# Kernel optimization log

Measured on AMD Instinct MI355X. Metric: run time of the kernel, lower is better.

## Reference

```python
import jax, jax.numpy as jnp
import numpy as np

N = 12288
IN_DIM = 256
HID = 64
E = 393216


def _gcn_edges(edge_index, n):
    # add self-loops, compute symmetric normalization (PyG GCNConv default)
    src = jnp.concatenate([edge_index[0], jnp.arange(n, dtype=edge_index.dtype)])
    dst = jnp.concatenate([edge_index[1], jnp.arange(n, dtype=edge_index.dtype)])
    deg = jax.ops.segment_sum(jnp.ones_like(src, dtype=jnp.float32), dst, num_segments=n)
    dinv = jnp.where(deg > 0, jax.lax.rsqrt(deg), 0.0)
    norm = dinv[src] * dinv[dst]  # [E+N]
    return src, dst, norm


def _conv(h, src, dst, norm, W, b, n):
    # GCNConv: linear transform then normalized sparse aggregation
    h = h @ W
    agg = jax.ops.segment_sum(h[src] * norm[:, None], dst, num_segments=n)
    return agg + b


def setup_inputs() -> dict:
    key = jax.random.key(0)
    ks = jax.random.split(key, 16)
    x = jax.random.normal(ks[0], (N, IN_DIM), dtype=jnp.float32)
    edge_index = jax.random.randint(ks[1], (2, E), 0, N, dtype=jnp.int32)
    s = 0.05
    p = {
        'enc_W1': jax.random.normal(ks[2], (IN_DIM, HID), jnp.float32) * s,
        'enc_b1': jnp.zeros((HID,), jnp.float32),
        'enc_W2': jax.random.normal(ks[3], (HID, HID), jnp.float32) * s,
        'enc_b2': jnp.zeros((HID,), jnp.float32),
        'd1_W1': jax.random.normal(ks[4], (HID // 2, HID), jnp.float32) * s,
        'd1_b1': jnp.zeros((HID,), jnp.float32),
        'd1_W2': jax.random.normal(ks[5], (HID, IN_DIM), jnp.float32) * s,
        'd1_b2': jnp.zeros((IN_DIM,), jnp.float32),
        'd2_W1': jax.random.normal(ks[6], (HID // 2, HID), jnp.float32) * s,
        'd2_b1': jnp.zeros((HID,), jnp.float32),
        'd2_W2': jax.random.normal(ks[7], (HID, IN_DIM), jnp.float32) * s,
        'd2_b2': jnp.zeros((IN_DIM,), jnp.float32),
        's_W': jax.random.normal(ks[8], (HID // 2, HID), jnp.float32) * s,
        's_b': jnp.zeros((HID,), jnp.float32),
    }
    return dict(x=x, edge_index=edge_index, **p)


def reference(x, edge_index, enc_W1, enc_b1, enc_W2, enc_b2,
              d1_W1, d1_b1, d1_W2, d1_b2, d2_W1, d2_b1, d2_W2, d2_b2,
              s_W, s_b):
    n = x.shape[0]
    src, dst, norm = _gcn_edges(edge_index, n)

    def encoder(h):
        h = jax.nn.relu(_conv(h, src, dst, norm, enc_W1, enc_b1, n))
        return _conv(h, src, dst, norm, enc_W2, enc_b2, n)

    def dec1(h):
        h = jax.nn.relu(_conv(h, src, dst, norm, d1_W1, d1_b1, n))
        return _conv(h, src, dst, norm, d1_W2, d1_b2, n)

    def dec2(h):
        h = jax.nn.relu(_conv(h, src, dst, norm, d2_W1, d2_b1, n))
        return _conv(h, src, dst, norm, d2_W2, d2_b2, n)

    z = encoder(x)
    # counterfactual: flip sensitive attribute (column 0)
    x_cf = x.at[:, 0].set(1.0 - x[:, 0])
    z_cf = encoder(x_cf)

    h = z.shape[1] // 2
    z_s, z_ns = z[:, :h], z[:, h:]
    z_s_cf = z_cf[:, :h]

    x_s_hat = dec1(z_s)
    x_ns_hat = dec2(z_ns)
    x_s_cf_hat = dec1(z_s_cf)

    # DotProductDecoder: 1-layer GCN then dense inner-product decode (sigmoid_s=False)
    hs = _conv(z_ns, src, dst, norm, s_W, s_b, n)
    s_ = hs @ hs.T  # [N, N]

    return (z_s, z_ns, x_s_hat, x_ns_hat, x_s_cf_hat, s_)
```

## Files before the change

### kernel.cpp

```cpp
#include <hip/hip_runtime.h>

#define N_NODES 12288
#define IN_DIM_ 256
#define HID_ 64
#define E_EDGES 393216
#define TOT_EDGES (E_EDGES + N_NODES)

typedef __attribute__((ext_vector_type(8))) short bf16x8;
typedef __attribute__((ext_vector_type(16))) float f32x16;

__device__ inline unsigned short f2bf_rne(float f) {
  unsigned int u = __float_as_uint(f);
  unsigned int r = u + 0x7fffu + ((u >> 16) & 1u);
  return (unsigned short)(r >> 16);
}
__device__ inline float bf2f(unsigned short h) {
  return __uint_as_float(((unsigned int)h) << 16);
}


__global__ __launch_bounds__(256) void k_init(const float* __restrict__ x,
                                              int* __restrict__ deg,
                                              float* __restrict__ coef) {
  int i = blockIdx.x * 256 + threadIdx.x;
  if (i < N_NODES) {
    deg[i] = 1;
    coef[i] = 1.0f - 2.0f * x[(size_t)i * IN_DIM_];
  }
}

__global__ __launch_bounds__(256) void k_count(const int* __restrict__ dst,
                                               int* __restrict__ deg) {
  int e = blockIdx.x * 256 + threadIdx.x;
  if (e < E_EDGES) atomicAdd(&deg[dst[e]], 1);
}

__global__ __launch_bounds__(1024) void k_scan(const int* __restrict__ deg,
                                               int* __restrict__ rowptr,
                                               int* __restrict__ cursor,
                                               float* __restrict__ dinv) {
  __shared__ int sh[1024];
  const int t = threadIdx.x;
  int loc[12];
  int s = 0;
#pragma unroll
  for (int i = 0; i < 12; i++) {
    int d = deg[t * 12 + i];
    dinv[t * 12 + i] = 1.0f / sqrtf((float)d);
    loc[i] = s;
    s += d;
  }
  sh[t] = s;
  __syncthreads();
  for (int off = 1; off < 1024; off <<= 1) {
    int v = (t >= off) ? sh[t - off] : 0;
    __syncthreads();
    sh[t] += v;
    __syncthreads();
  }
  int base = sh[t] - s;
#pragma unroll
  for (int i = 0; i < 12; i++) {
    int v = base + loc[i];
    rowptr[t * 12 + i] = v;
    cursor[t * 12 + i] = v;
  }
  if (t == 1023) rowptr[N_NODES] = sh[1023];
}

__global__ __launch_bounds__(256) void k_fill(const int* __restrict__ src,
                                              const int* __restrict__ dst,
                                              const float* __restrict__ dinv,
                                              int* __restrict__ cursor,
                                              int* __restrict__ col,
                                              float* __restrict__ wgt) {
  int e = blockIdx.x * 256 + threadIdx.x;
  if (e < E_EDGES) {
    int s = src[e], d = dst[e];
    int pos = atomicAdd(&cursor[d], 1);
    col[pos] = s;
    wgt[pos] = dinv[s] * dinv[d];
  } else if (e < TOT_EDGES) {
    int i = e - E_EDGES;
    int pos = atomicAdd(&cursor[i], 1);
    col[pos] = i;
    float di = dinv[i];
    wgt[pos] = di * di;
  }
}


template <bool BIAS, bool RELU, bool SPLIT>
__global__ __launch_bounds__(256) void k_agg64(const float* __restrict__ in,
                                               const int* __restrict__ rowptr,
                                               const int* __restrict__ col,
                                               const float* __restrict__ wgt,
                                               const float* __restrict__ bias,
                                               float* __restrict__ out,
                                               float* __restrict__ out2) {
  const int lane = threadIdx.x & 63;
  int node = blockIdx.x * 4 + (threadIdx.x >> 6);
  node = __builtin_amdgcn_readfirstlane(node);
  const int start = rowptr[node];
  const int end = rowptr[node + 1];
  float a0 = 0.0f, a1 = 0.0f, a2 = 0.0f, a3 = 0.0f;
  int e = start;
  for (; e + 8 <= end; e += 8) {
    int c0 = col[e + 0], c1 = col[e + 1], c2 = col[e + 2], c3 = col[e + 3];
    int c4 = col[e + 4], c5 = col[e + 5], c6 = col[e + 6], c7 = col[e + 7];
    float w0 = wgt[e + 0], w1 = wgt[e + 1], w2 = wgt[e + 2], w3 = wgt[e + 3];
    float w4 = wgt[e + 4], w5 = wgt[e + 5], w6 = wgt[e + 6], w7 = wgt[e + 7];
    float v0 = in[(size_t)c0 * 64 + lane];
    float v1 = in[(size_t)c1 * 64 + lane];
    float v2 = in[(size_t)c2 * 64 + lane];
    float v3 = in[(size_t)c3 * 64 + lane];
    float v4 = in[(size_t)c4 * 64 + lane];
    float v5 = in[(size_t)c5 * 64 + lane];
    float v6 = in[(size_t)c6 * 64 + lane];
    float v7 = in[(size_t)c7 * 64 + lane];
    a0 = fmaf(w0, v0, a0);
    a1 = fmaf(w1, v1, a1);
    a2 = fmaf(w2, v2, a2);
    a3 = fmaf(w3, v3, a3);
    a0 = fmaf(w4, v4, a0);
    a1 = fmaf(w5, v5, a1);
    a2 = fmaf(w6, v6, a2);
    a3 = fmaf(w7, v7, a3);
  }
  for (; e < end; ++e) {
    int c = col[e];
    a0 = fmaf(wgt[e], in[(size_t)c * 64 + lane], a0);
  }
  float acc = (a0 + a1) + (a2 + a3);
  if (BIAS) acc += bias[lane];
  if (RELU) acc = fmaxf(acc, 0.0f);
  if (SPLIT) {
    if (lane < 32)
      out[(size_t)node * 32 + lane] = acc;
    else
      out2[(size_t)node * 32 + (lane - 32)] = acc;
  } else {
    out[(size_t)node * 64 + lane] = acc;
  }
}

__global__ __launch_bounds__(256) void k_agg64_enc(
    const float* __restrict__ in, const int* __restrict__ rowptr,
    const int* __restrict__ col, const float* __restrict__ wgt,
    const float* __restrict__ bias, const float* __restrict__ coef,
    const float* __restrict__ wrow, float* __restrict__ out0,
    float* __restrict__ out1) {
  const int lane = threadIdx.x & 63;
  int node = blockIdx.x * 4 + (threadIdx.x >> 6);
  node = __builtin_amdgcn_readfirstlane(node);
  const int slice = blockIdx.y;
  const float wr = slice ? wrow[lane] : 0.0f;
  const int start = rowptr[node];
  const int end = rowptr[node + 1];
  float a0 = 0.0f, a1 = 0.0f, a2 = 0.0f, a3 = 0.0f;
  int e = start;
  for (; e + 8 <= end; e += 8) {
    int c0 = col[e + 0], c1 = col[e + 1], c2 = col[e + 2], c3 = col[e + 3];
    int c4 = col[e + 4], c5 = col[e + 5], c6 = col[e + 6], c7 = col[e + 7];
    float w0 = wgt[e + 0], w1 = wgt[e + 1], w2 = wgt[e + 2], w3 = wgt[e + 3];
    float w4 = wgt[e + 4], w5 = wgt[e + 5], w6 = wgt[e + 6], w7 = wgt[e + 7];
    float v0 = in[(size_t)c0 * 64 + lane];
    float v1 = in[(size_t)c1 * 64 + lane];
    float v2 = in[(size_t)c2 * 64 + lane];
    float v3 = in[(size_t)c3 * 64 + lane];
    float v4 = in[(size_t)c4 * 64 + lane];
    float v5 = in[(size_t)c5 * 64 + lane];
    float v6 = in[(size_t)c6 * 64 + lane];
    float v7 = in[(size_t)c7 * 64 + lane];
    v0 = fmaf(coef[c0], wr, v0);
    v1 = fmaf(coef[c1], wr, v1);
    v2 = fmaf(coef[c2], wr, v2);
    v3 = fmaf(coef[c3], wr, v3);
    v4 = fmaf(coef[c4], wr, v4);
    v5 = fmaf(coef[c5], wr, v5);
    v6 = fmaf(coef[c6], wr, v6);
    v7 = fmaf(coef[c7], wr, v7);
    a0 = fmaf(w0, v0, a0);
    a1 = fmaf(w1, v1, a1);
    a2 = fmaf(w2, v2, a2);
    a3 = fmaf(w3, v3, a3);
    a0 = fmaf(w4, v4, a0);
    a1 = fmaf(w5, v5, a1);
    a2 = fmaf(w6, v6, a2);
    a3 = fmaf(w7, v7, a3);
  }
  for (; e < end; ++e) {
    int c = col[e];
    float v = in[(size_t)c * 64 + lane];
    v = fmaf(coef[c], wr, v);
    a0 = fmaf(wgt[e], v, a0);
  }
  float acc = (a0 + a1) + (a2 + a3) + bias[lane];
  acc = fmaxf(acc, 0.0f);
  (slice ? out1 : out0)[(size_t)node * 64 + lane] = acc;
}

__global__ __launch_bounds__(256) void k_agg64_dec3(
    const float* __restrict__ in0, const float* __restrict__ in1,
    const float* __restrict__ in2, const int* __restrict__ rowptr,
    const int* __restrict__ col, const float* __restrict__ wgt,
    float* __restrict__ out0, float* __restrict__ out1,
    float* __restrict__ out2) {
  const int lane = threadIdx.x & 63;
  int node = blockIdx.x * 4 + (threadIdx.x >> 6);
  node = __builtin_amdgcn_readfirstlane(node);
  const int slice = blockIdx.y;
  const float* __restrict__ in = slice == 0 ? in0 : (slice == 1 ? in1 : in2);
  float* __restrict__ out = slice == 0 ? out0 : (slice == 1 ? out1 : out2);
  const int start = rowptr[node];
  const int end = rowptr[node + 1];
  float a0 = 0.0f, a1 = 0.0f, a2 = 0.0f, a3 = 0.0f;
  int e = start;
  for (; e + 8 <= end; e += 8) {
    int c0 = col[e + 0], c1 = col[e + 1], c2 = col[e + 2], c3 = col[e + 3];
    int c4 = col[e + 4], c5 = col[e + 5], c6 = col[e + 6], c7 = col[e + 7];
    float w0 = wgt[e + 0], w1 = wgt[e + 1], w2 = wgt[e + 2], w3 = wgt[e + 3];
    float w4 = wgt[e + 4], w5 = wgt[e + 5], w6 = wgt[e + 6], w7 = wgt[e + 7];
    float v0 = in[(size_t)c0 * 64 + lane];
    float v1 = in[(size_t)c1 * 64 + lane];
    float v2 = in[(size_t)c2 * 64 + lane];
    float v3 = in[(size_t)c3 * 64 + lane];
    float v4 = in[(size_t)c4 * 64 + lane];
    float v5 = in[(size_t)c5 * 64 + lane];
    float v6 = in[(size_t)c6 * 64 + lane];
    float v7 = in[(size_t)c7 * 64 + lane];
    a0 = fmaf(w0, v0, a0);
    a1 = fmaf(w1, v1, a1);
    a2 = fmaf(w2, v2, a2);
    a3 = fmaf(w3, v3, a3);
    a0 = fmaf(w4, v4, a0);
    a1 = fmaf(w5, v5, a1);
    a2 = fmaf(w6, v6, a2);
    a3 = fmaf(w7, v7, a3);
  }
  for (; e < end; ++e) {
    int c = col[e];
    a0 = fmaf(wgt[e], in[(size_t)c * 64 + lane], a0);
  }
  float acc = (a0 + a1) + (a2 + a3);
  out[(size_t)node * 64 + lane] = acc;
}

template <bool BIAS>
__global__ __launch_bounds__(256) void k_agg32(const float* __restrict__ in,
                                               const int* __restrict__ rowptr,
                                               const int* __restrict__ col,
                                               const float* __restrict__ wgt,
                                               const float* __restrict__ bias,
                                               float* __restrict__ out) {
  const int lane = threadIdx.x & 31;
  const int node = blockIdx.x * 8 + (threadIdx.x >> 5);
  const int start = rowptr[node];
  const int end = rowptr[node + 1];
  float a0 = 0.0f, a1 = 0.0f, a2 = 0.0f, a3 = 0.0f;
  int e = start;
  for (; e + 8 <= end; e += 8) {
    int c0 = col[e + 0], c1 = col[e + 1], c2 = col[e + 2], c3 = col[e + 3];
    int c4 = col[e + 4], c5 = col[e + 5], c6 = col[e + 6], c7 = col[e + 7];
    float w0 = wgt[e + 0], w1 = wgt[e + 1], w2 = wgt[e + 2], w3 = wgt[e + 3];
    float w4 = wgt[e + 4], w5 = wgt[e + 5], w6 = wgt[e + 6], w7 = wgt[e + 7];
    a0 = fmaf(w0, in[(size_t)c0 * 32 + lane], a0);
    a1 = fmaf(w1, in[(size_t)c1 * 32 + lane], a1);
    a2 = fmaf(w2, in[(size_t)c2 * 32 + lane], a2);
    a3 = fmaf(w3, in[(size_t)c3 * 32 + lane], a3);
    a0 = fmaf(w4, in[(size_t)c4 * 32 + lane], a0);
    a1 = fmaf(w5, in[(size_t)c5 * 32 + lane], a1);
    a2 = fmaf(w6, in[(size_t)c6 * 32 + lane], a2);
    a3 = fmaf(w7, in[(size_t)c7 * 32 + lane], a3);
  }
  for (; e < end; ++e) a0 = fmaf(wgt[e], in[(size_t)col[e] * 32 + lane], a0);
  float acc = (a0 + a1) + (a2 + a3);
  if (BIAS) acc += bias[lane];
  out[(size_t)node * 32 + lane] = acc;
}

__global__ __launch_bounds__(256) void k_agg32_b3(
    const float* __restrict__ in0, const float* __restrict__ in1,
    const float* __restrict__ in2, const int* __restrict__ rowptr,
    const int* __restrict__ col, const float* __restrict__ wgt,
    float* __restrict__ out0, float* __restrict__ out1,
    float* __restrict__ out2) {
  const int lane = threadIdx.x & 31;
  const int node = blockIdx.x * 8 + (threadIdx.x >> 5);
  const int slice = blockIdx.y;
  const float* __restrict__ in = slice == 0 ? in0 : (slice == 1 ? in1 : in2);
  float* __restrict__ out = slice == 0 ? out0 : (slice == 1 ? out1 : out2);
  const int start = rowptr[node];
  const int end = rowptr[node + 1];
  float a0 = 0.0f, a1 = 0.0f, a2 = 0.0f, a3 = 0.0f;
  int e = start;
  for (; e + 8 <= end; e += 8) {
    int c0 = col[e + 0], c1 = col[e + 1], c2 = col[e + 2], c3 = col[e + 3];
    int c4 = col[e + 4], c5 = col[e + 5], c6 = col[e + 6], c7 = col[e + 7];
    float w0 = wgt[e + 0], w1 = wgt[e + 1], w2 = wgt[e + 2], w3 = wgt[e + 3];
    float w4 = wgt[e + 4], w5 = wgt[e + 5], w6 = wgt[e + 6], w7 = wgt[e + 7];
    a0 = fmaf(w0, in[(size_t)c0 * 32 + lane], a0);
    a1 = fmaf(w1, in[(size_t)c1 * 32 + lane], a1);
    a2 = fmaf(w2, in[(size_t)c2 * 32 + lane], a2);
    a3 = fmaf(w3, in[(size_t)c3 * 32 + lane], a3);
    a0 = fmaf(w4, in[(size_t)c4 * 32 + lane], a0);
    a1 = fmaf(w5, in[(size_t)c5 * 32 + lane], a1);
    a2 = fmaf(w6, in[(size_t)c6 * 32 + lane], a2);
    a3 = fmaf(w7, in[(size_t)c7 * 32 + lane], a3);
  }
  for (; e < end; ++e) a0 = fmaf(wgt[e], in[(size_t)col[e] * 32 + lane], a0);
  out[(size_t)node * 32 + lane] = (a0 + a1) + (a2 + a3);
}


template <int K, int NF, int LDW, int RPT, bool BIAS, bool RELU>
__global__ __launch_bounds__(256) void k_gemm(const float* __restrict__ A,
                                              const float* __restrict__ W,
                                              const float* __restrict__ bias,
                                              float* __restrict__ C) {
  __shared__ float Ws[K * NF];
  for (int i = threadIdx.x; i < K * NF; i += 256) {
    int k = i / NF, c2 = i % NF;
    Ws[i] = W[k * LDW + c2];
  }
  __syncthreads();
  constexpr int G = 256 / NF;
  const int c = threadIdx.x % NF;
  const int rg = threadIdx.x / NF;
  const int r0 = blockIdx.x * (G * RPT) + rg * RPT;
  float acc[RPT];
#pragma unroll
  for (int i = 0; i < RPT; i++) acc[i] = 0.0f;
#pragma unroll 4
  for (int k = 0; k < K; ++k) {
    float wv = Ws[k * NF + c];
#pragma unroll
    for (int i = 0; i < RPT; i++)
      acc[i] = fmaf(A[(size_t)(r0 + i) * K + k], wv, acc[i]);
  }
  float b = BIAS ? bias[c] : 0.0f;
#pragma unroll
  for (int i = 0; i < RPT; i++) {
    float v = acc[i] + b;
    if (RELU) v = fmaxf(v, 0.0f);
    C[(size_t)(r0 + i) * NF + c] = v;
  }
}

__global__ __launch_bounds__(256) void k_gemm_enc2(
    const float* __restrict__ A0, const float* __restrict__ A1,
    const float* __restrict__ W, float* __restrict__ C0,
    float* __restrict__ C1) {
  __shared__ float Ws[64 * 64];
  const int slice = blockIdx.y;
  const float* __restrict__ A = slice ? A1 : A0;
  for (int i = threadIdx.x; i < 64 * 64; i += 256) Ws[i] = W[i];
  __syncthreads();
  const int c = threadIdx.x & 63;
  const int rg = threadIdx.x >> 6;
  const int r0 = blockIdx.x * 32 + rg * 8;
  float acc[8];
#pragma unroll
  for (int i = 0; i < 8; i++) acc[i] = 0.0f;
#pragma unroll 4
  for (int k = 0; k < 64; ++k) {
    float wv = Ws[k * 64 + c];
#pragma unroll
    for (int i = 0; i < 8; i++)
      acc[i] = fmaf(A[(size_t)(r0 + i) * 64 + k], wv, acc[i]);
  }
  if (slice == 0) {
#pragma unroll
    for (int i = 0; i < 8; i++) C0[(size_t)(r0 + i) * 64 + c] = acc[i];
  } else if (c < 32) {
#pragma unroll
    for (int i = 0; i < 8; i++) C1[(size_t)(r0 + i) * 32 + c] = acc[i];
  }
}

__global__ __launch_bounds__(256) void k_gemm_u3(
    const float* __restrict__ A0, const float* __restrict__ A1,
    const float* __restrict__ A2, const float* __restrict__ W0,
    const float* __restrict__ W1, const float* __restrict__ W2,
    const float* __restrict__ b0, const float* __restrict__ b1,
    const float* __restrict__ b2, float* __restrict__ C0,
    float* __restrict__ C1, float* __restrict__ C2) {
  __shared__ float Ws[32 * 64];
  const int slice = blockIdx.y;
  const float* __restrict__ A = slice == 0 ? A0 : (slice == 1 ? A1 : A2);
  const float* __restrict__ W = slice == 0 ? W0 : (slice == 1 ? W1 : W2);
  const float* __restrict__ bias = slice == 0 ? b0 : (slice == 1 ? b1 : b2);
  float* __restrict__ C = slice == 0 ? C0 : (slice == 1 ? C1 : C2);
  for (int i = threadIdx.x; i < 32 * 64; i += 256) Ws[i] = W[i];
  __syncthreads();
  const int c = threadIdx.x & 63;
  const int rg = threadIdx.x >> 6;
  const int r0 = blockIdx.x * 32 + rg * 8;
  float acc[8];
#pragma unroll
  for (int i = 0; i < 8; i++) acc[i] = 0.0f;
#pragma unroll 4
  for (int k = 0; k < 32; ++k) {
    float wv = Ws[k * 64 + c];
#pragma unroll
    for (int i = 0; i < 8; i++)
      acc[i] = fmaf(A[(size_t)(r0 + i) * 32 + k], wv, acc[i]);
  }
  float b = bias[c];
#pragma unroll
  for (int i = 0; i < 8; i++) {
    float v = acc[i] + b;
    C[(size_t)(r0 + i) * 64 + c] = fmaxf(v, 0.0f);
  }
}

__global__ __launch_bounds__(256) void k_gemm_o3(
    const float* __restrict__ A0, const float* __restrict__ A1,
    const float* __restrict__ A2, const float* __restrict__ W0,
    const float* __restrict__ W1, const float* __restrict__ W2,
    const float* __restrict__ b0, const float* __restrict__ b1,
    const float* __restrict__ b2, float* __restrict__ C0,
    float* __restrict__ C1, float* __restrict__ C2) {
  __shared__ float Ws[64 * 256];
  const int slice = blockIdx.y;
  const float* __restrict__ A = slice == 0 ? A0 : (slice == 1 ? A1 : A2);
  const float* __restrict__ W = slice == 0 ? W0 : (slice == 1 ? W1 : W2);
  const float* __restrict__ bias = slice == 0 ? b0 : (slice == 1 ? b1 : b2);
  float* __restrict__ C = slice == 0 ? C0 : (slice == 1 ? C1 : C2);
  for (int i = threadIdx.x; i < 64 * 256; i += 256) Ws[i] = W[i];
  __syncthreads();
  const int c = threadIdx.x;
  const int r0 = blockIdx.x * 8;
  float acc[8];
#pragma unroll
  for (int i = 0; i < 8; i++) acc[i] = 0.0f;
#pragma unroll 4
  for (int k = 0; k < 64; ++k) {
    float wv = Ws[k * 256 + c];
#pragma unroll
    for (int i = 0; i < 8; i++)
      acc[i] = fmaf(A[(size_t)(r0 + i) * 64 + k], wv, acc[i]);
  }
  float b = bias[c];
#pragma unroll
  for (int i = 0; i < 8; i++) C[(size_t)(r0 + i) * 256 + c] = acc[i] + b;
}

__global__ __launch_bounds__(256) void k_gemm_hs(const float* __restrict__ A,
                                                 const float* __restrict__ W,
                                                 const float* __restrict__ bias,
                                                 unsigned short* __restrict__ hi,
                                                 unsigned short* __restrict__ lo) {
  __shared__ float Ws[32 * 64];
  for (int i = threadIdx.x; i < 32 * 64; i += 256) {
    int k = i / 64, c2 = i % 64;
    Ws[i] = W[k * 64 + c2];
  }
  __syncthreads();
  const int c = threadIdx.x % 64;
  const int rg = threadIdx.x / 64;
  const int r0 = blockIdx.x * 32 + rg * 8;
  float acc[8];
#pragma unroll
  for (int i = 0; i < 8; i++) acc[i] = 0.0f;
#pragma unroll 4
  for (int k = 0; k < 32; ++k) {
    float wv = Ws[k * 64 + c];
#pragma unroll
    for (int i = 0; i < 8; i++)
      acc[i] = fmaf(A[(size_t)(r0 + i) * 32 + k], wv, acc[i]);
  }
  float b = bias[c];
#pragma unroll
  for (int i = 0; i < 8; i++) {
    float v = acc[i] + b;
    unsigned short h = f2bf_rne(v);
    float l = v - bf2f(h);
    hi[(size_t)(r0 + i) * 64 + c] = h;
    lo[(size_t)(r0 + i) * 64 + c] = f2bf_rne(l);
  }
}


__global__ __launch_bounds__(256) void k_syrk_mfma(
    const unsigned short* __restrict__ hhi, const unsigned short* __restrict__ hlo,
    float* __restrict__ out) {
  const int tid = threadIdx.x;
  const int lane = tid & 63;
  const int wave = tid >> 6;
  const int wy = wave >> 1, wx = wave & 1;
  const int m = lane & 31;
  const int koff = (lane >> 5) * 8;
  const size_t rb = (size_t)blockIdx.y * 128 + wy * 64;
  const size_t cb = (size_t)blockIdx.x * 128 + wx * 64;
  f32x16 acc[2][2];
#pragma unroll
  for (int i = 0; i < 2; i++)
#pragma unroll
    for (int j = 0; j < 2; j++) acc[i][j] = (f32x16)(0.0f);
#pragma unroll
  for (int k0 = 0; k0 < 64; k0 += 16) {
    bf16x8 ah[2], al[2], bh[2], bl[2];
#pragma unroll
    for (int t = 0; t < 2; t++) {
      size_t ra = (rb + t * 32 + m) * 64 + k0 + koff;
      ah[t] = *(const bf16x8*)(hhi + ra);
      al[t] = *(const bf16x8*)(hlo + ra);
      size_t rc = (cb + t * 32 + m) * 64 + k0 + koff;
      bh[t] = *(const bf16x8*)(hhi + rc);
      bl[t] = *(const bf16x8*)(hlo + rc);
    }
#pragma unroll
    for (int i = 0; i < 2; i++)
#pragma unroll
      for (int j = 0; j < 2; j++) {
        acc[i][j] = __builtin_amdgcn_mfma_f32_32x32x16_bf16(ah[i], bh[j], acc[i][j], 0, 0, 0);
        acc[i][j] = __builtin_amdgcn_mfma_f32_32x32x16_bf16(ah[i], bl[j], acc[i][j], 0, 0, 0);
        acc[i][j] = __builtin_amdgcn_mfma_f32_32x32x16_bf16(al[i], bh[j], acc[i][j], 0, 0, 0);
      }
  }
  const int rowoff = 4 * (lane >> 5);
  const int colc = lane & 31;
#pragma unroll
  for (int i = 0; i < 2; i++)
#pragma unroll
    for (int j = 0; j < 2; j++)
#pragma unroll
      for (int r = 0; r < 16; r++) {
        size_t row = rb + i * 32 + (r & 3) + 8 * (r >> 2) + rowoff;
        out[row * 12288 + cb + j * 32 + colc] = acc[i][j][r];
      }
}


extern "C" void kernel_launch(void* const* d_in, const int* in_sizes, int n_in,
                              void* d_out, int out_size, void* d_ws,
                              size_t ws_size, hipStream_t stream) {
  (void)in_sizes; (void)n_in; (void)out_size; (void)ws_size;
  const float* x = (const float*)d_in[0];
  const int* ei = (const int*)d_in[1];
  const int* src = ei;
  const int* dst = ei + E_EDGES;
  const float* eW1 = (const float*)d_in[2];
  const float* eb1 = (const float*)d_in[3];
  const float* eW2 = (const float*)d_in[4];
  const float* eb2 = (const float*)d_in[5];
  const float* d1W1 = (const float*)d_in[6];
  const float* d1b1 = (const float*)d_in[7];
  const float* d1W2 = (const float*)d_in[8];
  const float* d1b2 = (const float*)d_in[9];
  const float* d2W1 = (const float*)d_in[10];
  const float* d2b1 = (const float*)d_in[11];
  const float* d2W2 = (const float*)d_in[12];
  const float* d2b2 = (const float*)d_in[13];
  const float* sW = (const float*)d_in[14];
  const float* sb = (const float*)d_in[15];

  float* out = (float*)d_out;
  float* out_zs = out;
  float* out_zns = out + 393216;
  float* out_xs = out + 786432;
  float* out_xns = out + 3932160;
  float* out_xscf = out + 7077888;
  float* out_s = out + 10223616;

  char* w = (char*)d_ws;
  size_t o = 0;
  auto alloc = [&](size_t bytes) -> void* {
    void* p = (void*)(w + o);
    o += (bytes + 255) & ~(size_t)255;
    return p;
  };
  int* deg = (int*)alloc(N_NODES * 4);
  int* rowptr = (int*)alloc((N_NODES + 1) * 4);
  int* cursor = (int*)alloc(N_NODES * 4);
  int* col = (int*)alloc(TOT_EDGES * 4);
  float* wgt = (float*)alloc(TOT_EDGES * 4);
  float* dinv = (float*)alloc(N_NODES * 4);
  float* coef = (float*)alloc(N_NODES * 4);
  const size_t B64 = (size_t)N_NODES * 64 * 4;
  const size_t B32 = (size_t)N_NODES * 32 * 4;
  float* slotA = (float*)alloc(B64);
  float* slotB = (float*)alloc(B64);
  float* slotC = (float*)alloc(B64);
  float* slotU3 = (float*)alloc(B64);
  float* slotG2 = (float*)alloc(B64);
  float* slotG3 = (float*)alloc(B64);
  float* t32 = (float*)alloc(B32);
  float* zscf = (float*)alloc(B32);
  float* gs = (float*)alloc(B32);
  float* gscf = (float*)alloc(B32);
  float* gns = (float*)alloc(B32);
  unsigned short* hhi = (unsigned short*)alloc((size_t)N_NODES * 64 * 2);
  unsigned short* hlo = (unsigned short*)alloc((size_t)N_NODES * 64 * 2);

  k_init<<<48, 256, 0, stream>>>(x, deg, coef);
  k_count<<<1536, 256, 0, stream>>>(dst, deg);
  k_scan<<<1, 1024, 0, stream>>>(deg, rowptr, cursor, dinv);
  k_fill<<<1584, 256, 0, stream>>>(src, dst, dinv, cursor, col, wgt);

  k_gemm<256, 64, 64, 8, false, false><<<384, 256, 0, stream>>>(x, eW1, nullptr, slotA);
  k_agg64_enc<<<dim3(3072, 2), 256, 0, stream>>>(slotA, rowptr, col, wgt, eb1,
                                                 coef, eW1, slotB, slotC);
  k_gemm_enc2<<<dim3(384, 2), 256, 0, stream>>>(slotB, slotC, eW2, slotA, t32);
  k_agg64<true, false, true><<<3072, 256, 0, stream>>>(slotA, rowptr, col, wgt,
                                                       eb2, out_zs, out_zns);
  k_agg32<true><<<1536, 256, 0, stream>>>(t32, rowptr, col, wgt, eb2, zscf);

  k_agg32_b3<<<dim3(1536, 3), 256, 0, stream>>>(out_zs, zscf, out_zns, rowptr,
                                                col, wgt, gs, gscf, gns);
  k_gemm_hs<<<384, 256, 0, stream>>>(gns, sW, sb, hhi, hlo);
  k_gemm_u3<<<dim3(384, 3), 256, 0, stream>>>(gs, gscf, gns, d1W1, d1W1, d2W1,
                                              d1b1, d1b1, d2b1, slotB, slotC,
                                              slotU3);
  k_agg64_dec3<<<dim3(3072, 3), 256, 0, stream>>>(slotB, slotC, slotU3, rowptr,
                                                  col, wgt, slotA, slotG2,
                                                  slotG3);
  k_gemm_o3<<<dim3(1536, 3), 256, 0, stream>>>(slotA, slotG2, slotG3, d1W2,
                                               d1W2, d2W2, d1b2, d1b2, d2b2,
                                               out_xs, out_xscf, out_xns);

  k_syrk_mfma<<<dim3(96, 96), 256, 0, stream>>>(hhi, hlo, out_s);
}
```

Before: 999.0 us.

## Fuse small aggregation and GEMM launches and vectorize GEMM A-loads with float4

Merges the 64-wide and 32-wide encoder output aggregations into one two-slice kernel, and folds the hs projection GEMM into the decoder first-layer GEMM as a fourth slice. Together these remove kernel launches and the gaps between them. The dense GEMMs are rewritten to read A rows as float4, use fewer rows per thread with more blocks, and stage weights in smaller K-chunks, which cuts shared memory for the output GEMM. Occupancy and load efficiency may improve, at the cost of more blocks and extra synchronisation per K-chunk.

```diff
diff --git a/kernel.cpp b/kernel.cpp
--- a/kernel.cpp
+++ b/kernel.cpp
@@ -89,60 +89,6 @@
   }
 }
 
-
-template <bool BIAS, bool RELU, bool SPLIT>
-__global__ __launch_bounds__(256) void k_agg64(const float* __restrict__ in,
-                                               const int* __restrict__ rowptr,
-                                               const int* __restrict__ col,
-                                               const float* __restrict__ wgt,
-                                               const float* __restrict__ bias,
-                                               float* __restrict__ out,
-                                               float* __restrict__ out2) {
-  const int lane = threadIdx.x & 63;
-  int node = blockIdx.x * 4 + (threadIdx.x >> 6);
-  node = __builtin_amdgcn_readfirstlane(node);
-  const int start = rowptr[node];
-  const int end = rowptr[node + 1];
-  float a0 = 0.0f, a1 = 0.0f, a2 = 0.0f, a3 = 0.0f;
-  int e = start;
-  for (; e + 8 <= end; e += 8) {
-    int c0 = col[e + 0], c1 = col[e + 1], c2 = col[e + 2], c3 = col[e + 3];
-    int c4 = col[e + 4], c5 = col[e + 5], c6 = col[e + 6], c7 = col[e + 7];
-    float w0 = wgt[e + 0], w1 = wgt[e + 1], w2 = wgt[e + 2], w3 = wgt[e + 3];
-    float w4 = wgt[e + 4], w5 = wgt[e + 5], w6 = wgt[e + 6], w7 = wgt[e + 7];
-    float v0 = in[(size_t)c0 * 64 + lane];
-    float v1 = in[(size_t)c1 * 64 + lane];
-    float v2 = in[(size_t)c2 * 64 + lane];
-    float v3 = in[(size_t)c3 * 64 + lane];
-    float v4 = in[(size_t)c4 * 64 + lane];
-    float v5 = in[(size_t)c5 * 64 + lane];
-    float v6 = in[(size_t)c6 * 64 + lane];
-    float v7 = in[(size_t)c7 * 64 + lane];
-    a0 = fmaf(w0, v0, a0);
-    a1 = fmaf(w1, v1, a1);
-    a2 = fmaf(w2, v2, a2);
-    a3 = fmaf(w3, v3, a3);
-    a0 = fmaf(w4, v4, a0);
-    a1 = fmaf(w5, v5, a1);
-    a2 = fmaf(w6, v6, a2);
-    a3 = fmaf(w7, v7, a3);
-  }
-  for (; e < end; ++e) {
-    int c = col[e];
-    a0 = fmaf(wgt[e], in[(size_t)c * 64 + lane], a0);
-  }
-  float acc = (a0 + a1) + (a2 + a3);
-  if (BIAS) acc += bias[lane];
-  if (RELU) acc = fmaxf(acc, 0.0f);
-  if (SPLIT) {
-    if (lane < 32)
-      out[(size_t)node * 32 + lane] = acc;
-    else
-      out2[(size_t)node * 32 + (lane - 32)] = acc;
-  } else {
-    out[(size_t)node * 64 + lane] = acc;
-  }
-}
 
 __global__ __launch_bounds__(256) void k_agg64_enc(
     const float* __restrict__ in, const int* __restrict__ rowptr,
@@ -200,6 +146,79 @@
   (slice ? out1 : out0)[(size_t)node * 64 + lane] = acc;
 }
 
+__global__ __launch_bounds__(256) void k_agg_z(
+    const float* __restrict__ in64, const float* __restrict__ in32,
+    const int* __restrict__ rowptr, const int* __restrict__ col,
+    const float* __restrict__ wgt, const float* __restrict__ bias,
+    float* __restrict__ out_zs, float* __restrict__ out_zns,
+    float* __restrict__ out_zscf) {
+  if (blockIdx.y == 0) {
+    const int lane = threadIdx.x & 63;
+    int node = blockIdx.x * 4 + (threadIdx.x >> 6);
+    node = __builtin_amdgcn_readfirstlane(node);
+    const int start = rowptr[node];
+    const int end = rowptr[node + 1];
+    float a0 = 0.0f, a1 = 0.0f, a2 = 0.0f, a3 = 0.0f;
+    int e = start;
+    for (; e + 8 <= end; e += 8) {
+      int c0 = col[e + 0], c1 = col[e + 1], c2 = col[e + 2], c3 = col[e + 3];
+      int c4 = col[e + 4], c5 = col[e + 5], c6 = col[e + 6], c7 = col[e + 7];
+      float w0 = wgt[e + 0], w1 = wgt[e + 1], w2 = wgt[e + 2], w3 = wgt[e + 3];
+      float w4 = wgt[e + 4], w5 = wgt[e + 5], w6 = wgt[e + 6], w7 = wgt[e + 7];
+      float v0 = in64[(size_t)c0 * 64 + lane];
+      float v1 = in64[(size_t)c1 * 64 + lane];
+      float v2 = in64[(size_t)c2 * 64 + lane];
+      float v3 = in64[(size_t)c3 * 64 + lane];
+      float v4 = in64[(size_t)c4 * 64 + lane];
+      float v5 = in64[(size_t)c5 * 64 + lane];
+      float v6 = in64[(size_t)c6 * 64 + lane];
+      float v7 = in64[(size_t)c7 * 64 + lane];
+      a0 = fmaf(w0, v0, a0);
+      a1 = fmaf(w1, v1, a1);
+      a2 = fmaf(w2, v2, a2);
+      a3 = fmaf(w3, v3, a3);
+      a0 = fmaf(w4, v4, a0);
+      a1 = fmaf(w5, v5, a1);
+      a2 = fmaf(w6, v6, a2);
+      a3 = fmaf(w7, v7, a3);
+    }
+    for (; e < end; ++e) {
+      int c = col[e];
+      a0 = fmaf(wgt[e], in64[(size_t)c * 64 + lane], a0);
+    }
+    float acc = (a0 + a1) + (a2 + a3) + bias[lane];
+    if (lane < 32)
+      out_zs[(size_t)node * 32 + lane] = acc;
+    else
+      out_zns[(size_t)node * 32 + (lane - 32)] = acc;
+  } else {
+    if (blockIdx.x >= 1536) return;
+    const int lane = threadIdx.x & 31;
+    const int node = blockIdx.x * 8 + (threadIdx.x >> 5);
+    const int start = rowptr[node];
+    const int end = rowptr[node + 1];
+    float a0 = 0.0f, a1 = 0.0f, a2 = 0.0f, a3 = 0.0f;
+    int e = start;
+    for (; e + 8 <= end; e += 8) {
+      int c0 = col[e + 0], c1 = col[e + 1], c2 = col[e + 2], c3 = col[e + 3];
+      int c4 = col[e + 4], c5 = col[e + 5], c6 = col[e + 6], c7 = col[e + 7];
+      float w0 = wgt[e + 0], w1 = wgt[e + 1], w2 = wgt[e + 2], w3 = wgt[e + 3];
+      float w4 = wgt[e + 4], w5 = wgt[e + 5], w6 = wgt[e + 6], w7 = wgt[e + 7];
+      a0 = fmaf(w0, in32[(size_t)c0 * 32 + lane], a0);
+      a1 = fmaf(w1, in32[(size_t)c1 * 32 + lane], a1);
+      a2 = fmaf(w2, in32[(size_t)c2 * 32 + lane], a2);
+      a3 = fmaf(w3, in32[(size_t)c3 * 32 + lane], a3);
+      a0 = fmaf(w4, in32[(size_t)c4 * 32 + lane], a0);
+      a1 = fmaf(w5, in32[(size_t)c5 * 32 + lane], a1);
+      a2 = fmaf(w6, in32[(size_t)c6 * 32 + lane], a2);
+      a3 = fmaf(w7, in32[(size_t)c7 * 32 + lane], a3);
+    }
+    for (; e < end; ++e)
+      a0 = fmaf(wgt[e], in32[(size_t)col[e] * 32 + lane], a0);
+    out_zscf[(size_t)node * 32 + lane] = (a0 + a1) + (a2 + a3) + bias[lane];
+  }
+}
+
 __global__ __launch_bounds__(256) void k_agg64_dec3(
     const float* __restrict__ in0, const float* __restrict__ in1,
     const float* __restrict__ in2, const int* __restrict__ rowptr,
@@ -246,39 +265,6 @@
   out[(size_t)node * 64 + lane] = acc;
 }
 
-template <bool BIAS>
-__global__ __launch_bounds__(256) void k_agg32(const float* __restrict__ in,
-                                               const int* __restrict__ rowptr,
-                                               const int* __restrict__ col,
-                                               const float* __restrict__ wgt,
-                                               const float* __restrict__ bias,
-                                               float* __restrict__ out) {
-  const int lane = threadIdx.x & 31;
-  const int node = blockIdx.x * 8 + (threadIdx.x >> 5);
-  const int start = rowptr[node];
-  const int end = rowptr[node + 1];
-  float a0 = 0.0f, a1 = 0.0f, a2 = 0.0f, a3 = 0.0f;
-  int e = start;
-  for (; e + 8 <= end; e += 8) {
-    int c0 = col[e + 0], c1 = col[e + 1], c2 = col[e + 2], c3 = col[e + 3];
-    int c4 = col[e + 4], c5 = col[e + 5], c6 = col[e + 6], c7 = col[e + 7];
-    float w0 = wgt[e + 0], w1 = wgt[e + 1], w2 = wgt[e + 2], w3 = wgt[e + 3];
-    float w4 = wgt[e + 4], w5 = wgt[e + 5], w6 = wgt[e + 6], w7 = wgt[e + 7];
-    a0 = fmaf(w0, in[(size_t)c0 * 32 + lane], a0);
-    a1 = fmaf(w1, in[(size_t)c1 * 32 + lane], a1);
-    a2 = fmaf(w2, in[(size_t)c2 * 32 + lane], a2);
-    a3 = fmaf(w3, in[(size_t)c3 * 32 + lane], a3);
-    a0 = fmaf(w4, in[(size_t)c4 * 32 + lane], a0);
-    a1 = fmaf(w5, in[(size_t)c5 * 32 + lane], a1);
-    a2 = fmaf(w6, in[(size_t)c6 * 32 + lane], a2);
-    a3 = fmaf(w7, in[(size_t)c7 * 32 + lane], a3);
-  }
-  for (; e < end; ++e) a0 = fmaf(wgt[e], in[(size_t)col[e] * 32 + lane], a0);
-  float acc = (a0 + a1) + (a2 + a3);
-  if (BIAS) acc += bias[lane];
-  out[(size_t)node * 32 + lane] = acc;
-}
-
 __global__ __launch_bounds__(256) void k_agg32_b3(
     const float* __restrict__ in0, const float* __restrict__ in1,
     const float* __restrict__ in2, const int* __restrict__ rowptr,
@@ -313,17 +299,12 @@
 }
 
 
-template <int K, int NF, int LDW, int RPT, bool BIAS, bool RELU>
-__global__ __launch_bounds__(256) void k_gemm(const float* __restrict__ A,
-                                              const float* __restrict__ W,
-                                              const float* __restrict__ bias,
-                                              float* __restrict__ C) {
-  __shared__ float Ws[K * NF];
-  for (int i = threadIdx.x; i < K * NF; i += 256) {
-    int k = i / NF, c2 = i % NF;
-    Ws[i] = W[k * LDW + c2];
-  }
-  __syncthreads();
+template <int K, int KC, int NF, int LDW, int RPT, bool BIAS, bool RELU>
+__global__ __launch_bounds__(256) void k_gemm_v4(const float* __restrict__ A,
+                                                 const float* __restrict__ W,
+                                                 const float* __restrict__ bias,
+                                                 float* __restrict__ C) {
+  __shared__ float Ws[KC * NF];
   constexpr int G = 256 / NF;
   const int c = threadIdx.x % NF;
   const int rg = threadIdx.x / NF;
@@ -331,12 +312,29 @@
   float acc[RPT];
 #pragma unroll
   for (int i = 0; i < RPT; i++) acc[i] = 0.0f;
-#pragma unroll 4
-  for (int k = 0; k < K; ++k) {
-    float wv = Ws[k * NF + c];
-#pragma unroll
-    for (int i = 0; i < RPT; i++)
-      acc[i] = fmaf(A[(size_t)(r0 + i) * K + k], wv, acc[i]);
+  for (int k0 = 0; k0 < K; k0 += KC) {
+    for (int t = threadIdx.x; t < KC * NF; t += 256)
+      Ws[t] = W[(k0 + t / NF) * LDW + (t % NF)];
+    __syncthreads();
+#pragma unroll 2
+    for (int k = 0; k < KC; k += 4) {
+      float4 a[RPT];
+#pragma unroll
+      for (int i = 0; i < RPT; i++)
+        a[i] = *(const float4*)&A[(size_t)(r0 + i) * K + k0 + k];
+      float w0 = Ws[(k + 0) * NF + c];
+      float w1 = Ws[(k + 1) * NF + c];
+      float w2 = Ws[(k + 2) * NF + c];
+      float w3 = Ws[(k + 3) * NF + c];
+#pragma unroll
+      for (int i = 0; i < RPT; i++) {
+        acc[i] = fmaf(a[i].x, w0, acc[i]);
+        acc[i] = fmaf(a[i].y, w1, acc[i]);
+        acc[i] = fmaf(a[i].z, w2, acc[i]);
+        acc[i] = fmaf(a[i].w, w3, acc[i]);
+      }
+    }
+    __syncthreads();
   }
   float b = BIAS ? bias[c] : 0.0f;
 #pragma unroll
@@ -358,59 +356,95 @@
   __syncthreads();
   const int c = threadIdx.x & 63;
   const int rg = threadIdx.x >> 6;
-  const int r0 = blockIdx.x * 32 + rg * 8;
-  float acc[8];
-#pragma unroll
-  for (int i = 0; i < 8; i++) acc[i] = 0.0f;
-#pragma unroll 4
-  for (int k = 0; k < 64; ++k) {
-    float wv = Ws[k * 64 + c];
-#pragma unroll
-    for (int i = 0; i < 8; i++)
-      acc[i] = fmaf(A[(size_t)(r0 + i) * 64 + k], wv, acc[i]);
+  const int r0 = blockIdx.x * 16 + rg * 4;
+  float acc[4];
+#pragma unroll
+  for (int i = 0; i < 4; i++) acc[i] = 0.0f;
+#pragma unroll 2
+  for (int k = 0; k < 64; k += 4) {
+    float4 a[4];
+#pragma unroll
+    for (int i = 0; i < 4; i++)
+      a[i] = *(const float4*)&A[(size_t)(r0 + i) * 64 + k];
+    float w0 = Ws[(k + 0) * 64 + c];
+    float w1 = Ws[(k + 1) * 64 + c];
+    float w2 = Ws[(k + 2) * 64 + c];
+    float w3 = Ws[(k + 3) * 64 + c];
+#pragma unroll
+    for (int i = 0; i < 4; i++) {
+      acc[i] = fmaf(a[i].x, w0, acc[i]);
+      acc[i] = fmaf(a[i].y, w1, acc[i]);
+      acc[i] = fmaf(a[i].z, w2, acc[i]);
+      acc[i] = fmaf(a[i].w, w3, acc[i]);
+    }
   }
   if (slice == 0) {
 #pragma unroll
-    for (int i = 0; i < 8; i++) C0[(size_t)(r0 + i) * 64 + c] = acc[i];
+    for (int i = 0; i < 4; i++) C0[(size_t)(r0 + i) * 64 + c] = acc[i];
   } else if (c < 32) {
 #pragma unroll
-    for (int i = 0; i < 8; i++) C1[(size_t)(r0 + i) * 32 + c] = acc[i];
-  }
-}
-
-__global__ __launch_bounds__(256) void k_gemm_u3(
+    for (int i = 0; i < 4; i++) C1[(size_t)(r0 + i) * 32 + c] = acc[i];
+  }
+}
+
+__global__ __launch_bounds__(256) void k_gemm_u4(
     const float* __restrict__ A0, const float* __restrict__ A1,
     const float* __restrict__ A2, const float* __restrict__ W0,
     const float* __restrict__ W1, const float* __restrict__ W2,
-    const float* __restrict__ b0, const float* __restrict__ b1,
-    const float* __restrict__ b2, float* __restrict__ C0,
-    float* __restrict__ C1, float* __restrict__ C2) {
+    const float* __restrict__ W3, const float* __restrict__ b0,
+    const float* __restrict__ b1, const float* __restrict__ b2,
+    const float* __restrict__ b3, float* __restrict__ C0,
+    float* __restrict__ C1, float* __restrict__ C2,
+    unsigned short* __restrict__ hi, unsigned short* __restrict__ lo) {
   __shared__ float Ws[32 * 64];
   const int slice = blockIdx.y;
-  const float* __restrict__ A = slice == 0 ? A0 : (slice == 1 ? A1 : A2);
-  const float* __restrict__ W = slice == 0 ? W0 : (slice == 1 ? W1 : W2);
-  const float* __restrict__ bias = slice == 0 ? b0 : (slice == 1 ? b1 : b2);
-  float* __restrict__ C = slice == 0 ? C0 : (slice == 1 ? C1 : C2);
+  const float* __restrict__ A =
+      slice == 0 ? A0 : (slice == 1 ? A1 : A2);
+  const float* __restrict__ W =
+      slice == 0 ? W0 : (slice == 1 ? W1 : (slice == 2 ? W2 : W3));
+  const float* __restrict__ bias =
+      slice == 0 ? b0 : (slice == 1 ? b1 : (slice == 2 ? b2 : b3));
   for (int i = threadIdx.x; i < 32 * 64; i += 256) Ws[i] = W[i];
   __syncthreads();
   const int c = threadIdx.x & 63;
   const int rg = threadIdx.x >> 6;
-  const int r0 = blockIdx.x * 32 + rg * 8;
-  float acc[8];
-#pragma unroll
-  for (int i = 0; i < 8; i++) acc[i] = 0.0f;
-#pragma unroll 4
-  for (int k = 0; k < 32; ++k) {
-    float wv = Ws[k * 64 + c];
-#pragma unroll
-    for (int i = 0; i < 8; i++)
-      acc[i] = fmaf(A[(size_t)(r0 + i) * 32 + k], wv, acc[i]);
+  const int r0 = blockIdx.x * 16 + rg * 4;
+  float acc[4];
+#pragma unroll
+  for (int i = 0; i < 4; i++) acc[i] = 0.0f;
+#pragma unroll 2
+  for (int k = 0; k < 32; k += 4) {
+    float4 a[4];
+#pragma unroll
+    for (int i = 0; i < 4; i++)
+      a[i] = *(const float4*)&A[(size_t)(r0 + i) * 32 + k];
+    float w0 = Ws[(k + 0) * 64 + c];
+    float w1 = Ws[(k + 1) * 64 + c];
+    float w2 = Ws[(k + 2) * 64 + c];
+    float w3 = Ws[(k + 3) * 64 + c];
+#pragma unroll
+    for (int i = 0; i < 4; i++) {
+      acc[i] = fmaf(a[i].x, w0, acc[i]);
+      acc[i] = fmaf(a[i].y, w1, acc[i]);
+      acc[i] = fmaf(a[i].z, w2, acc[i]);
+      acc[i] = fmaf(a[i].w, w3, acc[i]);
+    }
   }
   float b = bias[c];
-#pragma unroll
-  for (int i = 0; i < 8; i++) {
-    float v = acc[i] + b;
-    C[(size_t)(r0 + i) * 64 + c] = fmaxf(v, 0.0f);
+  if (slice < 3) {
+    float* __restrict__ C = slice == 0 ? C0 : (slice == 1 ? C1 : C2);
+#pragma unroll
+    for (int i = 0; i < 4; i++)
+      C[(size_t)(r0 + i) * 64 + c] = fmaxf(acc[i] + b, 0.0f);
+  } else {
+#pragma unroll
+    for (int i = 0; i < 4; i++) {
+      float v = acc[i] + b;
+      unsigned short h = f2bf_rne(v);
+      float l = v - bf2f(h);
+      hi[(size_t)(r0 + i) * 64 + c] = h;
+      lo[(size_t)(r0 + i) * 64 + c] = f2bf_rne(l);
+    }
   }
 }
 
@@ -421,63 +455,56 @@
     const float* __restrict__ b0, const float* __restrict__ b1,
     const float* __restrict__ b2, float* __restrict__ C0,
     float* __restrict__ C1, float* __restrict__ C2) {
-  __shared__ float Ws[64 * 256];
+  __shared__ float Ws[16 * 256];
   const int slice = blockIdx.y;
   const float* __restrict__ A = slice == 0 ? A0 : (slice == 1 ? A1 : A2);
   const float* __restrict__ W = slice == 0 ? W0 : (slice == 1 ? W1 : W2);
   const float* __restrict__ bias = slice == 0 ? b0 : (slice == 1 ? b1 : b2);
   float* __restrict__ C = slice == 0 ? C0 : (slice == 1 ? C1 : C2);
-  for (int i = threadIdx.x; i < 64 * 256; i += 256) Ws[i] = W[i];
-  __syncthreads();
-  const int c = threadIdx.x;
-  const int r0 = blockIdx.x * 8;
-  float acc[8];
-#pragma unroll
-  for (int i = 0; i < 8; i++) acc[i] = 0.0f;
-#pragma unroll 4
-  for (int k = 0; k < 64; ++k) {
-    float wv = Ws[k * 256 + c];
-#pragma unroll
-    for (int i = 0; i < 8; i++)
-      acc[i] = fmaf(A[(size_t)(r0 + i) * 64 + k], wv, acc[i]);
-  }
-  float b = bias[c];
-#pragma unroll
-  for (int i = 0; i < 8; i++) C[(size_t)(r0 + i) * 256 + c] = acc[i] + b;
-}
-
-__global__ __launch_bounds__(256) void k_gemm_hs(const float* __restrict__ A,
-                                                 const float* __restrict__ W,
-                                                 const float* __restrict__ bias,
-                                                 unsigned short* __restrict__ hi,
-                                                 unsigned short* __restrict__ lo) {
-  __shared__ float Ws[32 * 64];
-  for (int i = threadIdx.x; i < 32 * 64; i += 256) {
-    int k = i / 64, c2 = i % 64;
-    Ws[i] = W[k * 64 + c2];
-  }
-  __syncthreads();
-  const int c = threadIdx.x % 64;
-  const int rg = threadIdx.x / 64;
-  const int r0 = blockIdx.x * 32 + rg * 8;
-  float acc[8];
-#pragma unroll
-  for (int i = 0; i < 8; i++) acc[i] = 0.0f;
-#pragma unroll 4
-  for (int k = 0; k < 32; ++k) {
-    float wv = Ws[k * 64 + c];
-#pragma unroll
-    for (int i = 0; i < 8; i++)
-      acc[i] = fmaf(A[(size_t)(r0 + i) * 32 + k], wv, acc[i]);
-  }
-  float b = bias[c];
-#pragma unroll
-  for (int i = 0; i < 8; i++) {
-    float v = acc[i] + b;
-    unsigned short h = f2bf_rne(v);
-    float l = v - bf2f(h);
-    hi[(size_t)(r0 + i) * 64 + c] = h;
-    lo[(size_t)(r0 + i) * 64 + c] = f2bf_rne(l);
+  const int c = threadIdx.x & 63;
+  const int rg = threadIdx.x >> 6;
+  const int r0 = blockIdx.x * 16 + rg * 4;
+  float acc[4][4];
+#pragma unroll
+  for (int i = 0; i < 4; i++)
+#pragma unroll
+    for (int j = 0; j < 4; j++) acc[i][j] = 0.0f;
+  for (int k0 = 0; k0 < 64; k0 += 16) {
+    for (int t = threadIdx.x; t < 16 * 256; t += 256)
+      Ws[t] = W[(k0 + (t >> 8)) * 256 + (t & 255)];
+    __syncthreads();
+#pragma unroll
+    for (int k = 0; k < 16; k += 4) {
+      float4 a[4];
+#pragma unroll
+      for (int i = 0; i < 4; i++)
+        a[i] = *(const float4*)&A[(size_t)(r0 + i) * 64 + k0 + k];
+#pragma unroll
+      for (int kk = 0; kk < 4; kk++) {
+        float w0 = Ws[(k + kk) * 256 + c];
+        float w1 = Ws[(k + kk) * 256 + c + 64];
+        float w2 = Ws[(k + kk) * 256 + c + 128];
+        float w3 = Ws[(k + kk) * 256 + c + 192];
+#pragma unroll
+        for (int i = 0; i < 4; i++) {
+          float av = kk == 0 ? a[i].x : (kk == 1 ? a[i].y : (kk == 2 ? a[i].z : a[i].w));
+          acc[i][0] = fmaf(av, w0, acc[i][0]);
+          acc[i][1] = fmaf(av, w1, acc[i][1]);
+          acc[i][2] = fmaf(av, w2, acc[i][2]);
+          acc[i][3] = fmaf(av, w3, acc[i][3]);
+        }
+      }
+    }
+    __syncthreads();
+  }
+  float bb0 = bias[c], bb1 = bias[c + 64], bb2 = bias[c + 128], bb3 = bias[c + 192];
+#pragma unroll
+  for (int i = 0; i < 4; i++) {
+    size_t base = (size_t)(r0 + i) * 256;
+    C[base + c] = acc[i][0] + bb0;
+    C[base + c + 64] = acc[i][1] + bb1;
+    C[base + c + 128] = acc[i][2] + bb2;
+    C[base + c + 192] = acc[i][3] + bb3;
   }
 }
 
@@ -599,26 +626,25 @@
   k_scan<<<1, 1024, 0, stream>>>(deg, rowptr, cursor, dinv);
   k_fill<<<1584, 256, 0, stream>>>(src, dst, dinv, cursor, col, wgt);
 
-  k_gemm<256, 64, 64, 8, false, false><<<384, 256, 0, stream>>>(x, eW1, nullptr, slotA);
+  k_gemm_v4<256, 64, 64, 64, 4, false, false><<<768, 256, 0, stream>>>(
+      x, eW1, nullptr, slotA);
   k_agg64_enc<<<dim3(3072, 2), 256, 0, stream>>>(slotA, rowptr, col, wgt, eb1,
                                                  coef, eW1, slotB, slotC);
-  k_gemm_enc2<<<dim3(384, 2), 256, 0, stream>>>(slotB, slotC, eW2, slotA, t32);
-  k_agg64<true, false, true><<<3072, 256, 0, stream>>>(slotA, rowptr, col, wgt,
-                                                       eb2, out_zs, out_zns);
-  k_agg32<true><<<1536, 256, 0, stream>>>(t32, rowptr, col, wgt, eb2, zscf);
+  k_gemm_enc2<<<dim3(768, 2), 256, 0, stream>>>(slotB, slotC, eW2, slotA, t32);
+  k_agg_z<<<dim3(3072, 2), 256, 0, stream>>>(slotA, t32, rowptr, col, wgt,
+                                             eb2, out_zs, out_zns, zscf);
 
   k_agg32_b3<<<dim3(1536, 3), 256, 0, stream>>>(out_zs, zscf, out_zns, rowptr,
                                                 col, wgt, gs, gscf, gns);
-  k_gemm_hs<<<384, 256, 0, stream>>>(gns, sW, sb, hhi, hlo);
-  k_gemm_u3<<<dim3(384, 3), 256, 0, stream>>>(gs, gscf, gns, d1W1, d1W1, d2W1,
-                                              d1b1, d1b1, d2b1, slotB, slotC,
-                                              slotU3);
+  k_gemm_u4<<<dim3(768, 4), 256, 0, stream>>>(gs, gscf, gns, d1W1, d1W1, d2W1,
+                                              sW, d1b1, d1b1, d2b1, sb, slotB,
+                                              slotC, slotU3, hhi, hlo);
   k_agg64_dec3<<<dim3(3072, 3), 256, 0, stream>>>(slotB, slotC, slotU3, rowptr,
                                                   col, wgt, slotA, slotG2,
                                                   slotG3);
-  k_gemm_o3<<<dim3(1536, 3), 256, 0, stream>>>(slotA, slotG2, slotG3, d1W2,
-                                               d1W2, d2W2, d1b2, d1b2, d2b2,
-                                               out_xs, out_xscf, out_xns);
+  k_gemm_o3<<<dim3(768, 3), 256, 0, stream>>>(slotA, slotG2, slotG3, d1W2,
+                                              d1W2, d2W2, d1b2, d1b2, d2b2,
+                                              out_xs, out_xscf, out_xns);
 
   k_syrk_mfma<<<dim3(96, 96), 256, 0, stream>>>(hhi, hlo, out_s);
 }
```

After: 988.0 us. About the same (-1.1%).
